# Kernel tuning notes

Measured on AMD Instinct MI355X. Metric: run time of the kernel, lower is better.

## Reference

```python
import jax, jax.numpy as jnp
import numpy as np

DIM = 320; HEADS = 8; DHEAD = 40; CTX_DIM = 768
INNER = HEADS * DHEAD; FF_INNER = 4 * DIM
B = 1; N = 4096; M = 77
SCALE = DHEAD ** -0.5


def setup_inputs() -> dict:
    key = jax.random.key(0)
    ks = jax.random.split(key, 16)
    p = lambda i, shape: jax.random.normal(ks[i], shape, dtype=jnp.float32) * 0.02
    return {
        "x": jax.random.normal(ks[0], (B, N, DIM), dtype=jnp.float32),
        "context": jax.random.normal(ks[1], (B, M, CTX_DIM), dtype=jnp.float32),
        "focused_attention_mask": jax.random.uniform(ks[2], (1, M, M), dtype=jnp.float32),
        "g1": jnp.ones((DIM,), jnp.float32), "b1": jnp.zeros((DIM,), jnp.float32),
        "g2": jnp.ones((DIM,), jnp.float32), "b2": jnp.zeros((DIM,), jnp.float32),
        "g3": jnp.ones((DIM,), jnp.float32), "b3": jnp.zeros((DIM,), jnp.float32),
        "Wq1": p(3, (DIM, INNER)), "Wk1": p(4, (DIM, INNER)), "Wv1": p(5, (DIM, INNER)),
        "Wo1": p(6, (INNER, DIM)), "bo1": jnp.zeros((DIM,), jnp.float32),
        "Wq2": p(7, (DIM, INNER)), "Wk2": p(8, (CTX_DIM, INNER)), "Wv2": p(9, (CTX_DIM, INNER)),
        "Wo2": p(10, (INNER, DIM)), "bo2": jnp.zeros((DIM,), jnp.float32),
        "Wff1": p(11, (DIM, 2 * FF_INNER)), "bff1": jnp.zeros((2 * FF_INNER,), jnp.float32),
        "Wff2": p(12, (FF_INNER, DIM)), "bff2": jnp.zeros((DIM,), jnp.float32),
        "use_fca": 1,
    }


def _ln(x, g, b):
    mu = x.mean(-1, keepdims=True)
    var = jnp.mean((x - mu) ** 2, -1, keepdims=True)
    return (x - mu) * jax.lax.rsqrt(var + 1e-5) * g + b


def _attn(xn, ctx, Wq, Wk, Wv, Wo, bo, fam, use_fca):
    b, n, _ = xn.shape
    heads = lambda t: t.reshape(b, t.shape[1], HEADS, DHEAD).transpose(0, 2, 1, 3)  # b h n d
    q, k, v = heads(xn @ Wq), heads(ctx @ Wk), heads(ctx @ Wv)
    sim = jnp.einsum('bhid,bhjd->bhij', q, k) * SCALE
    if use_fca:
        m = fam.shape[-1]  # fam: [1, m, m], batch must be 1 (repeat_interleave semantics)
        fw = jnp.einsum('bhqk,dk->bhqd', sim[..., :m], fam[0])
        fw = jnp.minimum(jnp.abs(fw), 1.0)
        fw = fw / (jnp.max(fw, axis=-1, keepdims=True) + 1e-6)
        fw = (fw > 0.6).astype(sim.dtype)
        sim = sim.at[..., :m].add((fw - 1.0) * 50.0)
    a = jax.nn.softmax(sim, axis=-1)
    o = jnp.einsum('bhij,bhjd->bhid', a, v).transpose(0, 2, 1, 3).reshape(b, n, INNER)
    return o @ Wo + bo


def reference(x, context, focused_attention_mask,
              g1, b1, g2, b2, g3, b3,
              Wq1, Wk1, Wv1, Wo1, bo1,
              Wq2, Wk2, Wv2, Wo2, bo2,
              Wff1, bff1, Wff2, bff2, use_fca):
    # attn1: self-attention (context=None in original -> use_fca forced to 0)
    h1 = _ln(x, g1, b1)
    x = _attn(h1, h1, Wq1, Wk1, Wv1, Wo1, bo1, None, 0) + x
    # attn2: cross-attention with focused-attention mask
    h2 = _ln(x, g2, b2)
    x = _attn(h2, context, Wq2, Wk2, Wv2, Wo2, bo2, focused_attention_mask, int(use_fca)) + x
    # GEGLU feed-forward
    h3 = _ln(x, g3, b3)
    proj = h3 @ Wff1 + bff1
    a_, gate = jnp.split(proj, 2, axis=-1)
    x = (a_ * jax.nn.gelu(gate, approximate=False)) @ Wff2 + bff2 + x
    return x
```

## Files before the change

kernel.cpp:

```cpp
#include <hip/hip_runtime.h>
#include <math.h>

typedef __bf16 bf16_t;
typedef __bf16 bf16x8 __attribute__((ext_vector_type(8)));
typedef __bf16 bf16x4 __attribute__((ext_vector_type(4)));
typedef float  f32x4  __attribute__((ext_vector_type(4)));
typedef _Float16 f16_t;
typedef _Float16 f16x4 __attribute__((ext_vector_type(4)));
typedef _Float16 f16x8 __attribute__((ext_vector_type(8)));
typedef __fp16 hf16x2 __attribute__((ext_vector_type(2)));

static constexpr float ATT_SCALE = 0.15811388300841897f;
static constexpr float SC2 = 0.22811031f;
static constexpr float LOG2E = 1.4426950408889634f;

__device__ __forceinline__ bf16_t f2b(float f) {
  unsigned u = __float_as_uint(f);
  u = (u + 0x7fffu + ((u >> 16) & 1u)) >> 16;
  unsigned short s = (unsigned short)u;
  bf16_t r;
  *(unsigned short*)&r = s;
  return r;
}
__device__ __forceinline__ float b2f(bf16_t b) {
  unsigned short s = *(const unsigned short*)&b;
  return __uint_as_float(((unsigned)s) << 16);
}
__device__ __forceinline__ void sto(float v, float* p)  { *p = v; }
__device__ __forceinline__ void sto(float v, bf16_t* p) { *p = f2b(v); }
__device__ __forceinline__ unsigned pkh2(float a, float b) {
  hf16x2 h = __builtin_amdgcn_cvt_pkrtz(a, b);
  return *(unsigned*)&h;
}
__device__ __forceinline__ void gl_lds16(const void* g, void* l) {
  __builtin_amdgcn_global_load_lds((const __attribute__((address_space(1))) unsigned*)g,
                                   (__attribute__((address_space(3))) unsigned*)l, 16, 0, 0);
}

__global__ __launch_bounds__(256) void prep_ln_kernel(
    const float* __restrict__ Wq1, const float* __restrict__ Wk1, const float* __restrict__ Wv1,
    const float* __restrict__ Wo1, const float* __restrict__ Wq2,
    const float* __restrict__ Wk2, const float* __restrict__ Wv2, const float* __restrict__ Wo2,
    const float* __restrict__ Wff1, const float* __restrict__ Wff2,
    const float* __restrict__ fam,
    bf16_t* __restrict__ wqkvt, bf16_t* __restrict__ wo1t, float* __restrict__ wkv2t,
    bf16_t* __restrict__ wo2t, bf16_t* __restrict__ wff1t, bf16_t* __restrict__ wff2t,
    bf16_t* __restrict__ wq2th, bf16_t* __restrict__ wq2tl,
    bf16_t* __restrict__ famh, bf16_t* __restrict__ faml,
    bf16_t* __restrict__ zpad,
    const float* __restrict__ x, const float* __restrict__ g1, const float* __restrict__ b1,
    bf16_t* __restrict__ h1b)
{
  const int b = blockIdx.x;
  const int tid = threadIdx.x;

  if (b >= 634) {
    const int bb = b - 634;
    const int lane = tid & 63;
    const int row = bb * 4 + (tid >> 6);
    const float* xr = x + (size_t)row * 320;
    float v[5], s = 0.f, s2 = 0.f;
#pragma unroll
    for (int i = 0; i < 5; i++) { v[i] = xr[lane + i*64]; s += v[i]; s2 += v[i]*v[i]; }
#pragma unroll
    for (int o = 32; o; o >>= 1) { s += __shfl_xor(s, o); s2 += __shfl_xor(s2, o); }
    float mu = s * (1.f/320.f);
    float rs = rsqrtf(fmaxf(s2*(1.f/320.f) - mu*mu, 0.f) + 1e-5f);
#pragma unroll
    for (int i = 0; i < 5; i++) {
      int c = lane + i*64;
      h1b[(size_t)row*320 + c] = f2b((v[i]-mu)*rs*g1[c] + b1[c]);
    }
    return;
  }

  if (b >= 570) {
    for (int idx = (b - 570)*256 + tid; idx < 9216 + 135168; idx += 64*256) {
      if (idx < 9216) {
        int d = idx / 96, k = idx - d*96;
        float v = (d < 77 && k < 77) ? fam[d*77 + k] : 0.f;
        bf16_t h = f2b(v);
        famh[idx] = h;
        faml[idx] = f2b(v - b2f(h));
      } else {
        zpad[idx - 9216] = f2b(0.f);
      }
    }
    return;
  }

  __shared__ float T[64][65];
  const float* src; int S, O, n0, k0, mode;
  float scale = 1.f;
  bf16_t* outb = nullptr; float* outf = nullptr;
  int nadj;

  if (b < 75) {
    int tn = b / 5, tk = b - tn*5;
    n0 = tn*64; k0 = tk*64; S = 320; O = 320; mode = 0; outb = wqkvt;
    if (n0 < 320)      { src = Wq1; nadj = n0;       scale = SC2; }
    else if (n0 < 640) { src = Wk1; nadj = n0 - 320; }
    else               { src = Wv1; nadj = n0 - 640; }
  } else if (b < 100) {
    int b2 = b - 75; int tn = b2 / 5, tk = b2 - tn*5;
    n0 = tn*64; k0 = tk*64; S = 320; O = 320; mode = 0; outb = wo1t; src = Wo1; nadj = n0;
  } else if (b < 220) {
    int b2 = b - 100; int tn = b2 / 12, tk = b2 - tn*12;
    n0 = tn*64; k0 = tk*64; S = 320; O = 768; mode = 1; outf = wkv2t;
    if (n0 < 320) { src = Wk2; nadj = n0; } else { src = Wv2; nadj = n0 - 320; }
  } else if (b < 245) {
    int b2 = b - 220; int tn = b2 / 5, tk = b2 - tn*5;
    n0 = tn*64; k0 = tk*64; S = 320; O = 320; mode = 0; outb = wo2t; src = Wo2; nadj = n0;
  } else if (b < 445) {
    int b2 = b - 245; int tn = b2 / 5, tk = b2 - tn*5;
    n0 = tn*64; k0 = tk*64; S = 2560; O = 320; mode = 0; outb = wff1t; src = Wff1; nadj = n0;
  } else if (b < 545) {
    int b2 = b - 445; int tn = b2 / 20, tk = b2 - tn*20;
    n0 = tn*64; k0 = tk*64; S = 320; O = 1280; mode = 0; outb = wff2t; src = Wff2; nadj = n0;
  } else {
    int b2 = b - 545; int tn = b2 / 5, tk = b2 - tn*5;
    n0 = tn*64; k0 = tk*64; S = 320; O = 320; mode = 2; src = Wq2; nadj = n0;
  }

  const int r4 = tid >> 6;
  const int c  = tid & 63;
  const float* srcp = src + nadj;
#pragma unroll
  for (int i = 0; i < 16; i++) {
    int r = i*4 + r4;
    T[c][r] = srcp[(size_t)(k0 + r)*S + c] * scale;
  }
  __syncthreads();
#pragma unroll
  for (int i = 0; i < 16; i++) {
    int r = i*4 + r4;
    float v = T[r][c];
    size_t oi = (size_t)(n0 + r)*O + k0 + c;
    if (mode == 0) {
      outb[oi] = f2b(v);
    } else if (mode == 1) {
      outf[oi] = v;
    } else {
      bf16_t h = f2b(v);
      wq2th[oi] = h;
      wq2tl[oi] = f2b(v - b2f(h));
    }
  }
}

template<typename OT>
__global__ __launch_bounds__(256) void ln_kernel(
    const float* __restrict__ x, const float* __restrict__ g, const float* __restrict__ b,
    OT* __restrict__ out)
{
  const int lane = threadIdx.x & 63;
  const int row = blockIdx.x * 4 + (threadIdx.x >> 6);
  const float* xr = x + (size_t)row * 320;
  float v[5], s = 0.f, s2 = 0.f;
#pragma unroll
  for (int i = 0; i < 5; i++) { v[i] = xr[lane + i*64]; s += v[i]; s2 += v[i]*v[i]; }
#pragma unroll
  for (int o = 32; o; o >>= 1) { s += __shfl_xor(s, o); s2 += __shfl_xor(s2, o); }
  float mu = s * (1.f/320.f);
  float rs = rsqrtf(fmaxf(s2*(1.f/320.f) - mu*mu, 0.f) + 1e-5f);
#pragma unroll
  for (int i = 0; i < 5; i++) {
    int c = lane + i*64;
    sto((v[i]-mu)*rs*g[c] + b[c], &out[(size_t)row*320 + c]);
  }
}

__global__ __launch_bounds__(256) void ln2_split_kernel(
    const float* __restrict__ x, const float* __restrict__ g, const float* __restrict__ b,
    bf16_t* __restrict__ hi, bf16_t* __restrict__ lo)
{
  const int lane = threadIdx.x & 63;
  const int row = blockIdx.x * 4 + (threadIdx.x >> 6);
  const float* xr = x + (size_t)row * 320;
  float v[5], s = 0.f, s2 = 0.f;
#pragma unroll
  for (int i = 0; i < 5; i++) { v[i] = xr[lane + i*64]; s += v[i]; s2 += v[i]*v[i]; }
#pragma unroll
  for (int o = 32; o; o >>= 1) { s += __shfl_xor(s, o); s2 += __shfl_xor(s2, o); }
  float mu = s * (1.f/320.f);
  float rs = rsqrtf(fmaxf(s2*(1.f/320.f) - mu*mu, 0.f) + 1e-5f);
#pragma unroll
  for (int i = 0; i < 5; i++) {
    int c = lane + i*64;
    float y = (v[i]-mu)*rs*g[c] + b[c];
    bf16_t h = f2b(y);
    hi[(size_t)row*320 + c] = h;
    lo[(size_t)row*320 + c] = f2b(y - b2f(h));
  }
}

__global__ __launch_bounds__(256) void kv2_dot_kernel(
    const float* __restrict__ ctx, const float* __restrict__ wkv2t,
    bf16_t* __restrict__ k2h, bf16_t* __restrict__ k2l, bf16_t* __restrict__ v2t)
{
  __shared__ float4 Bs[16][193];
  const int tid = threadIdx.x;
  const int nb = blockIdx.x % 40, ms = blockIdx.x / 40;
  const int n0 = nb*16;
  for (int e = tid; e < 16*192; e += 256) {
    int row = e / 192, c4 = e - row*192;
    Bs[row][c4] = *(const float4*)(wkv2t + (size_t)(n0+row)*768 + c4*4);
  }
  __syncthreads();
  const int g = tid >> 4, q = tid & 15;
  const int mlo = ms*20;
  const int mhi = (mlo + 20 > 77) ? 77 : mlo + 20;
  for (int m = mlo; m < mhi; m++) {
    const float4* a = (const float4*)(ctx + (size_t)m*768);
    float acc = 0.f;
#pragma unroll
    for (int i = 0; i < 12; i++) {
      float4 av = a[i*16+q], bv = Bs[g][i*16+q];
      acc += av.x*bv.x + av.y*bv.y + av.z*bv.z + av.w*bv.w;
    }
#pragma unroll
    for (int o = 8; o; o >>= 1) acc += __shfl_xor(acc, o);
    if (q == 0) {
      int n = n0 + g;
      if (n < 320) {
        int h = n / 40, d = n - h*40;
        int idx = h*6144 + m*64 + d;
        bf16_t hh = f2b(acc);
        k2h[idx] = hh;
        k2l[idx] = f2b(acc - b2f(hh));
      } else {
        int n2 = n - 320; int h = n2 / 40, d = n2 - h*40;
        v2t[h*4608 + d*96 + m] = f2b(acc);
      }
    }
  }
}

__global__ __launch_bounds__(256) void repack_vt_kernel(
    const bf16_t* __restrict__ qkvb, f16_t* __restrict__ vpack, bf16_t* __restrict__ kpack)
{
  __shared__ f16_t T[64*44];
  const int tid = threadIdx.x;
  const int t0 = blockIdx.x * 64, h = blockIdx.y;
  for (int e = tid; e < 320; e += 256) {
    int t = e / 5, c8 = (e - t*5) * 8;
    bf16x8 v = *(const bf16x8*)(qkvb + (size_t)(t0+t)*960 + 640 + h*40 + c8);
    f16_t* dst = &T[t*44 + c8];
#pragma unroll
    for (int j = 0; j < 8; j++) dst[j] = (f16_t)b2f(v[j]);
  }
  __syncthreads();
  for (int e = tid; e < 3072; e += 256) {
    int dt = e >> 10;
    int r  = e & 1023;
    int g2 = r >> 9, o = r & 511;
    int lane = o >> 3, j = o & 7;
    int qd = lane >> 4, ln = lane & 15;
    int d = dt*16 + ln;
    int key = g2*32 + ((j & 4) ? 16 : 0) + qd*4 + (j & 3);
    float val;
    if (d < 40)       val = (float)T[key*44 + d];
    else if (d == 40) val = 1.0f;
    else              val = 0.0f;
    vpack[(((size_t)h*3 + dt)*128 + (t0 >> 5) + g2)*512 + o] = (f16_t)val;
  }
  for (int e = tid; e < 2560; e += 256) {
    int g = e / 640, o = e - g*640;
    int key = t0 + g*16;
    bf16_t val;
    if (o < 512) {
      int lane = o >> 3, j = o & 7;
      int qd = lane >> 4, ln = lane & 15;
      val = qkvb[(size_t)(key + ln)*960 + 320 + h*40 + qd*8 + j];
    } else {
      int o2 = o - 512; int ln = o2 >> 3, j = o2 & 7;
      val = qkvb[(size_t)(key + ln)*960 + 320 + h*40 + 32 + j];
    }
    kpack[((size_t)h*256 + (t0 >> 4) + g)*640 + o] = val;
  }
}

__global__ __launch_bounds__(512, 4) void flash_self_kernel(
    const bf16_t* __restrict__ qkvb, const bf16_t* __restrict__ kpack,
    const f16_t* __restrict__ vpack,
    bf16_t* __restrict__ o1a)
{
  __shared__ float Red[12288];
  const int tid = threadIdx.x;
  const int w = tid >> 6, lane = tid & 63;
  const int ln = lane & 15, qd = lane >> 4;
  const int qh = w >> 2, kh = w & 3;
  const int h = blockIdx.x & 7;
  const int q0 = (blockIdx.x >> 3) * 64;

  const int kgbase = h*256 + kh*2;
  const int vgbase = h*384 + kh;
  const int lko = lane*8;

  bf16x8 zero8 = {};
  bf16x8 bq[2][2];
#pragma unroll
  for (int nt = 0; nt < 2; nt++) {
    const bf16_t* qp = qkvb + (size_t)(q0 + qh*32 + nt*16 + ln)*960 + h*40;
    bq[nt][0] = *(const bf16x8*)(qp + qd*8);
    bq[nt][1] = (qd == 0) ? *(const bf16x8*)(qp + 32) : zero8;
  }

  f32x4 zero4 = {0.f,0.f,0.f,0.f};
  f32x4 oacc[3][2];
#pragma unroll
  for (int a = 0; a < 3; a++)
#pragma unroll
    for (int b = 0; b < 2; b++) oacc[a][b] = zero4;

#define FS_LOADK(DST, K0)                                                       \
  {                                                                             \
    const bf16_t* kp_ = kpack + ((size_t)kgbase + ((K0) >> 4)) * 640;           \
    DST[0][0] = *(const bf16x8*)(kp_ + lko);                                    \
    DST[0][1] = (qd == 0) ? *(const bf16x8*)(kp_ + 512 + ln*8) : zero8;         \
    DST[1][0] = *(const bf16x8*)(kp_ + 640 + lko);                              \
    DST[1][1] = (qd == 0) ? *(const bf16x8*)(kp_ + 1152 + ln*8) : zero8;        \
  }

#define FS_LOADV(DST, K0)                                                       \
  {                                                                             \
    _Pragma("unroll")                                                           \
    for (int dt_ = 0; dt_ < 3; dt_++)                                           \
      DST[dt_] = *(const f16x8*)(vpack + ((size_t)vgbase + dt_*128 + ((K0) >> 5)) * 512 + lko); \
  }

#define FS_COMPUTE(KA, VA)                                                      \
  {                                                                             \
    __builtin_amdgcn_s_setprio(1);                                              \
    _Pragma("unroll")                                                           \
    for (int nt = 0; nt < 2; nt++) {                                            \
      f32x4 s0 = __builtin_amdgcn_mfma_f32_16x16x32_bf16(KA[0][0], bq[nt][0], zero4, 0,0,0); \
      s0 = __builtin_amdgcn_mfma_f32_16x16x32_bf16(KA[0][1], bq[nt][1], s0, 0,0,0); \
      f32x4 s1 = __builtin_amdgcn_mfma_f32_16x16x32_bf16(KA[1][0], bq[nt][0], zero4, 0,0,0); \
      s1 = __builtin_amdgcn_mfma_f32_16x16x32_bf16(KA[1][1], bq[nt][1], s1, 0,0,0); \
      uint4 u_;                                                                 \
      u_.x = pkh2(__builtin_amdgcn_exp2f(s0[0]), __builtin_amdgcn_exp2f(s0[1])); \
      u_.y = pkh2(__builtin_amdgcn_exp2f(s0[2]), __builtin_amdgcn_exp2f(s0[3])); \
      u_.z = pkh2(__builtin_amdgcn_exp2f(s1[0]), __builtin_amdgcn_exp2f(s1[1])); \
      u_.w = pkh2(__builtin_amdgcn_exp2f(s1[2]), __builtin_amdgcn_exp2f(s1[3])); \
      f16x8 pb = *(f16x8*)&u_;                                                  \
      _Pragma("unroll")                                                         \
      for (int dt = 0; dt < 3; dt++)                                            \
        oacc[dt][nt] = __builtin_amdgcn_mfma_f32_16x16x32_f16(VA[dt], pb, oacc[dt][nt], 0,0,0); \
    }                                                                           \
    __builtin_amdgcn_s_setprio(0);                                              \
  }

  bf16x8 ka[2][2], kb[2][2];
  f16x8 va[3], vb[3];
  FS_LOADK(ka, 0);
  FS_LOADV(va, 0);
#pragma unroll 1
  for (int it = 0; it < 32; it += 2) {
    const int k0 = it*128;
    FS_LOADK(kb, k0 + 128);
    FS_LOADV(vb, k0 + 128);
    FS_COMPUTE(ka, va);
    FS_LOADK(ka, (it + 2 < 32) ? (k0 + 256) : 0);
    FS_LOADV(va, (it + 2 < 32) ? (k0 + 256) : 0);
    FS_COMPUTE(kb, vb);
  }
#undef FS_LOADK
#undef FS_LOADV
#undef FS_COMPUTE

#pragma unroll
  for (int nt = 0; nt < 2; nt++)
#pragma unroll
    for (int dt = 0; dt < 3; dt++)
      *(f32x4*)&Red[((w*2 + nt)*3 + dt)*256 + ln*16 + qd*4] = oacc[dt][nt];
  __syncthreads();
  const int dgrp = tid & 7, lq = (tid >> 3) & 15, ntw = (tid >> 7) & 1, qh2 = tid >> 8;
  float l = Red[(((qh2*4 + 0)*2 + ntw)*3 + 2)*256 + lq*16 + 8]
          + Red[(((qh2*4 + 1)*2 + ntw)*3 + 2)*256 + lq*16 + 8]
          + Red[(((qh2*4 + 2)*2 + ntw)*3 + 2)*256 + lq*16 + 8]
          + Red[(((qh2*4 + 3)*2 + ntw)*3 + 2)*256 + lq*16 + 8];
  float inv = 1.f / l;
  bf16_t* obase = o1a + (size_t)(q0 + qh2*32 + ntw*16 + lq)*320 + h*40;
#pragma unroll
  for (int i = 0; i < 5; i++) {
    int d = dgrp + i*8;
    int dt = d >> 4, dr = d & 15;
    float o = Red[(((qh2*4 + 0)*2 + ntw)*3 + dt)*256 + lq*16 + dr]
            + Red[(((qh2*4 + 1)*2 + ntw)*3 + dt)*256 + lq*16 + dr]
            + Red[(((qh2*4 + 2)*2 + ntw)*3 + dt)*256 + lq*16 + dr]
            + Red[(((qh2*4 + 3)*2 + ntw)*3 + dt)*256 + lq*16 + dr];
    obase[d] = f2b(o * inv);
  }
}

__global__ __launch_bounds__(256) void attn_cross_kernel(
    const float* __restrict__ q2, const bf16_t* __restrict__ k2h, const bf16_t* __restrict__ k2l,
    const bf16_t* __restrict__ famh, const bf16_t* __restrict__ faml,
    const bf16_t* __restrict__ v2t, const int* __restrict__ use_fca,
    bf16_t* __restrict__ o2)
{
  __shared__ bf16_t SMh[4][16*96];
  __shared__ bf16_t SMl[4][16*96];
  __shared__ bf16_t PAs[4][16*96];
  const int tid = threadIdx.x;
  const int w = tid >> 6, lane = tid & 63;
  const int ln = lane & 15, qd = lane >> 4;
  const int h = blockIdx.x & 7;
  const int q0 = (blockIdx.x >> 3)*64 + w*16;
  const int fca = use_fca[0];
  bf16_t* smh = SMh[w];
  bf16_t* sml = SMl[w];
  bf16_t* pa  = PAs[w];

  {
    bf16x4 z = {};
    int q = lane >> 2, c = 80 + (lane & 3)*4;
    *(bf16x4*)&smh[q*96 + c] = z;
    *(bf16x4*)&sml[q*96 + c] = z;
    *(bf16x4*)&pa [q*96 + c] = z;
  }

  bf16x8 zero8 = {};
  bf16x8 aqh0, aql0, aqh1 = zero8, aql1 = zero8;
  {
    const float* qp = q2 + (size_t)(q0 + ln)*320 + h*40;
    float4 v0 = *(const float4*)(qp + qd*8);
    float4 v1 = *(const float4*)(qp + qd*8 + 4);
    float qv[8] = {v0.x,v0.y,v0.z,v0.w,v1.x,v1.y,v1.z,v1.w};
#pragma unroll
    for (int i = 0; i < 8; i++) {
      bf16_t hh = f2b(qv[i]);
      aqh0[i] = hh; aql0[i] = f2b(qv[i] - b2f(hh));
    }
    if (qd == 0) {
      float4 u0 = *(const float4*)(qp + 32);
      float4 u1 = *(const float4*)(qp + 36);
      float uv[8] = {u0.x,u0.y,u0.z,u0.w,u1.x,u1.y,u1.z,u1.w};
#pragma unroll
      for (int i = 0; i < 8; i++) {
        bf16_t hh = f2b(uv[i]);
        aqh1[i] = hh; aql1[i] = f2b(uv[i] - b2f(hh));
      }
    }
  }

  f32x4 zero4 = {0.f,0.f,0.f,0.f};
  float ss[5][4];
  __builtin_amdgcn_s_setprio(1);
#pragma unroll
  for (int nt = 0; nt < 5; nt++) {
    const bf16_t* kb = k2h + ((size_t)h*96 + nt*16 + ln)*64 + qd*8;
    const bf16_t* kl = k2l + ((size_t)h*96 + nt*16 + ln)*64 + qd*8;
    bf16x8 kh0 = *(const bf16x8*)kb;
    bf16x8 kh1 = *(const bf16x8*)(kb + 32);
    bf16x8 kl0 = *(const bf16x8*)kl;
    bf16x8 kl1 = *(const bf16x8*)(kl + 32);
    f32x4 s;
    s = __builtin_amdgcn_mfma_f32_16x16x32_bf16(aqh0, kl0, zero4, 0, 0, 0);
    s = __builtin_amdgcn_mfma_f32_16x16x32_bf16(aql0, kh0, s, 0, 0, 0);
    s = __builtin_amdgcn_mfma_f32_16x16x32_bf16(aqh0, kh0, s, 0, 0, 0);
    s = __builtin_amdgcn_mfma_f32_16x16x32_bf16(aqh1, kl1, s, 0, 0, 0);
    s = __builtin_amdgcn_mfma_f32_16x16x32_bf16(aql1, kh1, s, 0, 0, 0);
    s = __builtin_amdgcn_mfma_f32_16x16x32_bf16(aqh1, kh1, s, 0, 0, 0);
#pragma unroll
    for (int r = 0; r < 4; r++) {
      float sv = s[r] * ATT_SCALE;
      ss[nt][r] = sv;
      bf16_t hh = f2b(sv);
      smh[(qd*4 + r)*96 + nt*16 + ln] = hh;
      sml[(qd*4 + r)*96 + nt*16 + ln] = f2b(sv - b2f(hh));
    }
  }
  __builtin_amdgcn_s_setprio(0);

  f32x4 facc[5];
#pragma unroll
  for (int nt = 0; nt < 5; nt++) facc[nt] = zero4;
  __builtin_amdgcn_s_setprio(1);
#pragma unroll
  for (int c = 0; c < 3; c++) {
    bf16x8 sah = *(const bf16x8*)&smh[ln*96 + c*32 + qd*8];
    bf16x8 sal = *(const bf16x8*)&sml[ln*96 + c*32 + qd*8];
#pragma unroll
    for (int nt = 0; nt < 5; nt++) {
      bf16x8 fh8 = *(const bf16x8*)(famh + ((size_t)(nt*16 + ln))*96 + c*32 + qd*8);
      bf16x8 fl8 = *(const bf16x8*)(faml + ((size_t)(nt*16 + ln))*96 + c*32 + qd*8);
      facc[nt] = __builtin_amdgcn_mfma_f32_16x16x32_bf16(sah, fl8, facc[nt], 0, 0, 0);
      facc[nt] = __builtin_amdgcn_mfma_f32_16x16x32_bf16(sal, fh8, facc[nt], 0, 0, 0);
      facc[nt] = __builtin_amdgcn_mfma_f32_16x16x32_bf16(sah, fh8, facc[nt], 0, 0, 0);
    }
  }
  __builtin_amdgcn_s_setprio(0);

  float pr[5][4];
  if (fca) {
    float fwv[5][4], fm[4];
#pragma unroll
    for (int nt = 0; nt < 5; nt++)
#pragma unroll
      for (int r = 0; r < 4; r++) fwv[nt][r] = fminf(fabsf(facc[nt][r]), 1.f);
#pragma unroll
    for (int r = 0; r < 4; r++) {
      float m = fmaxf(fmaxf(fwv[0][r], fwv[1][r]), fmaxf(fwv[2][r], fmaxf(fwv[3][r], fwv[4][r])));
#pragma unroll
      for (int o = 8; o; o >>= 1) m = fmaxf(m, __shfl_xor(m, o));
      fm[r] = m;
    }
#pragma unroll
    for (int nt = 0; nt < 5; nt++)
#pragma unroll
      for (int r = 0; r < 4; r++) {
        float lg = ss[nt][r] - ((fwv[nt][r] > 0.6f*(fm[r] + 1e-6f)) ? 0.f : 50.f);
        pr[nt][r] = __builtin_amdgcn_exp2f(lg * LOG2E);
      }
  } else {
#pragma unroll
    for (int nt = 0; nt < 5; nt++)
#pragma unroll
      for (int r = 0; r < 4; r++)
        pr[nt][r] = __builtin_amdgcn_exp2f(ss[nt][r] * LOG2E);
  }
  if (ln >= 13) {
#pragma unroll
    for (int r = 0; r < 4; r++) pr[4][r] = 0.f;
  }
  float l_[4] = {0.f,0.f,0.f,0.f};
#pragma unroll
  for (int nt = 0; nt < 5; nt++)
#pragma unroll
    for (int r = 0; r < 4; r++) {
      l_[r] += pr[nt][r];
      pa[(qd*4 + r)*96 + nt*16 + ln] = f2b(pr[nt][r]);
    }
#pragma unroll
  for (int r = 0; r < 4; r++)
#pragma unroll
    for (int o = 8; o; o >>= 1) l_[r] += __shfl_xor(l_[r], o);

  f32x4 oacc[3];
#pragma unroll
  for (int nt = 0; nt < 3; nt++) oacc[nt] = zero4;
  __builtin_amdgcn_s_setprio(1);
#pragma unroll
  for (int c = 0; c < 3; c++) {
    bf16x8 paf = *(const bf16x8*)&pa[ln*96 + c*32 + qd*8];
#pragma unroll
    for (int nt = 0; nt < 3; nt++) {
      bf16x8 vb = *(const bf16x8*)(v2t + ((size_t)h*48 + nt*16 + ln)*96 + c*32 + qd*8);
      oacc[nt] = __builtin_amdgcn_mfma_f32_16x16x32_bf16(paf, vb, oacc[nt], 0, 0, 0);
    }
  }
  __builtin_amdgcn_s_setprio(0);
  float inv[4];
#pragma unroll
  for (int r = 0; r < 4; r++) inv[r] = 1.f / l_[r];
#pragma unroll
  for (int nt = 0; nt < 3; nt++) {
    int d = nt*16 + ln;
    if (d < 40) {
#pragma unroll
      for (int r = 0; r < 4; r++)
        o2[(size_t)(q0 + qd*4 + r)*320 + h*40 + d] = f2b(oacc[nt][r]*inv[r]);
    }
  }
}

template<int OUT_BF16>
__global__ __launch_bounds__(256) void gemm_bf16_kernel(
    const bf16_t* __restrict__ A, const bf16_t* __restrict__ Bt,
    const float* __restrict__ bias, const float* __restrict__ resid,
    void* __restrict__ Cout, int M, int N, int K)
{
  __shared__ __align__(16) bf16_t As[128][64];
  __shared__ __align__(16) bf16_t Bs[64][64];
  const int tid = threadIdx.x;
  const int m0 = blockIdx.x * 128, n0 = blockIdx.y * 64;
  const int w = tid >> 6, lane = tid & 63;
  const int wr = w >> 1, wc = w & 1;
  const int ln = lane & 15, qd = lane >> 4;
  const int lr = lane >> 3, lsw = (lane & 7) ^ lr;
  char* asb = (char*)&As[0][0];
  char* bsb = (char*)&Bs[0][0];
  f32x4 zero = {0.f, 0.f, 0.f, 0.f};
  f32x4 acc[4][2];
#pragma unroll
  for (int a = 0; a < 4; a++)
#pragma unroll
    for (int b = 0; b < 2; b++) acc[a][b] = zero;

  for (int k0 = 0; k0 < K; k0 += 64) {
    __syncthreads();
#pragma unroll
    for (int i = 0; i < 4; i++)
      gl_lds16(A + (size_t)(m0 + (i*4 + w)*8 + lr)*K + k0 + lsw*8, asb + (i*4 + w)*1024);
#pragma unroll
    for (int i = 0; i < 2; i++)
      gl_lds16(Bt + (size_t)(n0 + (i*4 + w)*8 + lr)*K + k0 + lsw*8, bsb + (i*4 + w)*1024);
    __syncthreads();
#pragma unroll
    for (int c = 0; c < 2; c++) {
      const int sa = (((c*4 + qd) ^ (ln & 7))) * 8;
      bf16x8 af[4], bfr[2];
#pragma unroll
      for (int mt = 0; mt < 4; mt++)
        af[mt] = *(const bf16x8*)&As[wr*64 + mt*16 + ln][sa];
#pragma unroll
      for (int nt = 0; nt < 2; nt++)
        bfr[nt] = *(const bf16x8*)&Bs[wc*32 + nt*16 + ln][sa];
#pragma unroll
      for (int mt = 0; mt < 4; mt++)
#pragma unroll
        for (int nt = 0; nt < 2; nt++)
          acc[mt][nt] = __builtin_amdgcn_mfma_f32_16x16x32_bf16(af[mt], bfr[nt], acc[mt][nt], 0, 0, 0);
    }
  }
#pragma unroll
  for (int mt = 0; mt < 4; mt++)
#pragma unroll
    for (int nt = 0; nt < 2; nt++)
#pragma unroll
      for (int r = 0; r < 4; r++) {
        int gm = m0 + wr*64 + mt*16 + qd*4 + r;
        int gn = n0 + wc*32 + nt*16 + ln;
        float v = acc[mt][nt][r];
        if (bias)  v += bias[gn];
        if (resid) v += resid[(size_t)gm*N + gn];
        if (OUT_BF16) sto(v, &((bf16_t*)Cout)[(size_t)gm*N + gn]);
        else          sto(v, &((float*)Cout)[(size_t)gm*N + gn]);
      }
}

template<int OUT_BF16>
__global__ __launch_bounds__(256) void gemm_bf16_32_kernel(
    const bf16_t* __restrict__ A, const bf16_t* __restrict__ Bt,
    const float* __restrict__ bias, const float* __restrict__ resid,
    void* __restrict__ Cout, int M, int N, int K)
{
  __shared__ __align__(16) bf16_t As[32][64];
  __shared__ __align__(16) bf16_t Bs[64][64];
  const int tid = threadIdx.x;
  const int m0 = blockIdx.x * 32, n0 = blockIdx.y * 64;
  const int w = tid >> 6, lane = tid & 63;
  const int wr = w >> 1, wc = w & 1;
  const int ln = lane & 15, qd = lane >> 4;
  const int lr = lane >> 3, lsw = (lane & 7) ^ lr;
  char* asb = (char*)&As[0][0];
  char* bsb = (char*)&Bs[0][0];
  f32x4 zero = {0.f, 0.f, 0.f, 0.f};
  f32x4 acc[2];
  acc[0] = zero; acc[1] = zero;

  for (int k0 = 0; k0 < K; k0 += 64) {
    __syncthreads();
    gl_lds16(A + (size_t)(m0 + w*8 + lr)*K + k0 + lsw*8, asb + w*1024);
#pragma unroll
    for (int i = 0; i < 2; i++)
      gl_lds16(Bt + (size_t)(n0 + (i*4 + w)*8 + lr)*K + k0 + lsw*8, bsb + (i*4 + w)*1024);
    __syncthreads();
#pragma unroll
    for (int c = 0; c < 2; c++) {
      const int sa = (((c*4 + qd) ^ (ln & 7))) * 8;
      bf16x8 af = *(const bf16x8*)&As[wr*16 + ln][sa];
#pragma unroll
      for (int nt = 0; nt < 2; nt++) {
        bf16x8 bfr = *(const bf16x8*)&Bs[wc*32 + nt*16 + ln][sa];
        acc[nt] = __builtin_amdgcn_mfma_f32_16x16x32_bf16(af, bfr, acc[nt], 0, 0, 0);
      }
    }
  }
#pragma unroll
  for (int nt = 0; nt < 2; nt++)
#pragma unroll
    for (int r = 0; r < 4; r++) {
      int gm = m0 + wr*16 + qd*4 + r;
      int gn = n0 + wc*32 + nt*16 + ln;
      float v = acc[nt][r];
      if (bias)  v += bias[gn];
      if (resid) v += resid[(size_t)gm*N + gn];
      if (OUT_BF16) sto(v, &((bf16_t*)Cout)[(size_t)gm*N + gn]);
      else          sto(v, &((float*)Cout)[(size_t)gm*N + gn]);
    }
}

__global__ __launch_bounds__(256) void gemm3_32_kernel(
    const bf16_t* __restrict__ Ah, const bf16_t* __restrict__ Al,
    const bf16_t* __restrict__ Bth, const bf16_t* __restrict__ Btl,
    float* __restrict__ C, int M, int N, int K)
{
  __shared__ bf16_t Ash[32][72];
  __shared__ bf16_t Asl[32][72];
  __shared__ bf16_t Bsh[64][72];
  __shared__ bf16_t Bsl[64][72];
  const int tid = threadIdx.x;
  const int m0 = blockIdx.x * 32, n0 = blockIdx.y * 64;
  const int w = tid >> 6, lane = tid & 63;
  const int wr = w >> 1, wc = w & 1;
  const int ln = lane & 15, qd = lane >> 4;
  f32x4 zero = {0.f, 0.f, 0.f, 0.f};
  f32x4 acc[2];
  acc[0] = zero; acc[1] = zero;

  for (int k0 = 0; k0 < K; k0 += 64) {
    __syncthreads();
    {
      int r = tid >> 3, c8 = (tid & 7) * 8;
      *(bf16x8*)&Ash[r][c8] = *(const bf16x8*)(Ah + (size_t)(m0+r)*K + k0 + c8);
      *(bf16x8*)&Asl[r][c8] = *(const bf16x8*)(Al + (size_t)(m0+r)*K + k0 + c8);
    }
#pragma unroll
    for (int i = 0; i < 2; i++) {
      int vid = tid + i*256;
      int r = vid >> 3, c8 = (vid & 7) * 8;
      *(bf16x8*)&Bsh[r][c8] = *(const bf16x8*)(Bth + (size_t)(n0+r)*K + k0 + c8);
      *(bf16x8*)&Bsl[r][c8] = *(const bf16x8*)(Btl + (size_t)(n0+r)*K + k0 + c8);
    }
    __syncthreads();
#pragma unroll
    for (int c = 0; c < 2; c++) {
      bf16x8 afh = *(const bf16x8*)&Ash[wr*16 + ln][c*32 + qd*8];
      bf16x8 afl = *(const bf16x8*)&Asl[wr*16 + ln][c*32 + qd*8];
#pragma unroll
      for (int nt = 0; nt < 2; nt++) {
        bf16x8 bfh = *(const bf16x8*)&Bsh[wc*32 + nt*16 + ln][c*32 + qd*8];
        bf16x8 bfl = *(const bf16x8*)&Bsl[wc*32 + nt*16 + ln][c*32 + qd*8];
        acc[nt] = __builtin_amdgcn_mfma_f32_16x16x32_bf16(afh, bfl, acc[nt], 0, 0, 0);
        acc[nt] = __builtin_amdgcn_mfma_f32_16x16x32_bf16(afl, bfh, acc[nt], 0, 0, 0);
        acc[nt] = __builtin_amdgcn_mfma_f32_16x16x32_bf16(afh, bfh, acc[nt], 0, 0, 0);
      }
    }
  }
#pragma unroll
  for (int nt = 0; nt < 2; nt++)
#pragma unroll
    for (int r = 0; r < 4; r++) {
      int gm = m0 + wr*16 + qd*4 + r;
      int gn = n0 + wc*32 + nt*16 + ln;
      C[(size_t)gm*N + gn] = acc[nt][r];
    }
}

__global__ __launch_bounds__(256) void gemm_geglu_kernel(
    const bf16_t* __restrict__ A, const bf16_t* __restrict__ Bt,
    const float* __restrict__ bias, bf16_t* __restrict__ gg, int K)
{
  __shared__ __align__(16) bf16_t As[128][64];
  __shared__ __align__(16) bf16_t Ba[64][64];
  __shared__ __align__(16) bf16_t Bg[64][64];
  const int tid = threadIdx.x;
  const int m0 = blockIdx.x * 128, n0 = blockIdx.y * 64;
  const int w = tid >> 6, lane = tid & 63;
  const int wr = w >> 1, wc = w & 1;
  const int ln = lane & 15, qd = lane >> 4;
  const int lr = lane >> 3, lsw = (lane & 7) ^ lr;
  char* asb = (char*)&As[0][0];
  char* bab = (char*)&Ba[0][0];
  char* bgb = (char*)&Bg[0][0];
  f32x4 zero = {0.f, 0.f, 0.f, 0.f};
  f32x4 acca[4][2], accg[4][2];
#pragma unroll
  for (int a = 0; a < 4; a++)
#pragma unroll
    for (int b = 0; b < 2; b++) { acca[a][b] = zero; accg[a][b] = zero; }

  for (int k0 = 0; k0 < K; k0 += 64) {
    __syncthreads();
#pragma unroll
    for (int i = 0; i < 4; i++)
      gl_lds16(A + (size_t)(m0 + (i*4 + w)*8 + lr)*K + k0 + lsw*8, asb + (i*4 + w)*1024);
#pragma unroll
    for (int i = 0; i < 2; i++) {
      gl_lds16(Bt + (size_t)(n0 + (i*4 + w)*8 + lr)*K + k0 + lsw*8, bab + (i*4 + w)*1024);
      gl_lds16(Bt + (size_t)(n0 + 1280 + (i*4 + w)*8 + lr)*K + k0 + lsw*8, bgb + (i*4 + w)*1024);
    }
    __syncthreads();
#pragma unroll
    for (int c = 0; c < 2; c++) {
      const int sa = (((c*4 + qd) ^ (ln & 7))) * 8;
      bf16x8 af[4], ba[2], bg[2];
#pragma unroll
      for (int mt = 0; mt < 4; mt++)
        af[mt] = *(const bf16x8*)&As[wr*64 + mt*16 + ln][sa];
#pragma unroll
      for (int nt = 0; nt < 2; nt++) {
        ba[nt] = *(const bf16x8*)&Ba[wc*32 + nt*16 + ln][sa];
        bg[nt] = *(const bf16x8*)&Bg[wc*32 + nt*16 + ln][sa];
      }
#pragma unroll
      for (int mt = 0; mt < 4; mt++)
#pragma unroll
        for (int nt = 0; nt < 2; nt++) {
          acca[mt][nt] = __builtin_amdgcn_mfma_f32_16x16x32_bf16(af[mt], ba[nt], acca[mt][nt], 0, 0, 0);
          accg[mt][nt] = __builtin_amdgcn_mfma_f32_16x16x32_bf16(af[mt], bg[nt], accg[mt][nt], 0, 0, 0);
        }
    }
  }
#pragma unroll
  for (int mt = 0; mt < 4; mt++)
#pragma unroll
    for (int nt = 0; nt < 2; nt++)
#pragma unroll
      for (int r = 0; r < 4; r++) {
        int gm = m0 + wr*64 + mt*16 + qd*4 + r;
        int gn = n0 + wc*32 + nt*16 + ln;
        float va = acca[mt][nt][r] + bias[gn];
        float vg = accg[mt][nt][r] + bias[1280 + gn];
        float ge = 0.5f * vg * (1.f + erff(vg * 0.70710678118654752f));
        gg[(size_t)gm*1280 + gn] = f2b(va * ge);
      }
}

extern "C" void kernel_launch(void* const* d_in, const int* in_sizes, int n_in,
                              void* d_out, int out_size, void* d_ws, size_t ws_size,
                              hipStream_t stream)
{
  const float* x    = (const float*)d_in[0];
  const float* ctx  = (const float*)d_in[1];
  const float* fam  = (const float*)d_in[2];
  const float* g1   = (const float*)d_in[3];
  const float* b1   = (const float*)d_in[4];
  const float* g2   = (const float*)d_in[5];
  const float* b2   = (const float*)d_in[6];
  const float* g3   = (const float*)d_in[7];
  const float* b3   = (const float*)d_in[8];
  const float* Wq1  = (const float*)d_in[9];
  const float* Wk1  = (const float*)d_in[10];
  const float* Wv1  = (const float*)d_in[11];
  const float* Wo1  = (const float*)d_in[12];
  const float* bo1  = (const float*)d_in[13];
  const float* Wq2  = (const float*)d_in[14];
  const float* Wk2  = (const float*)d_in[15];
  const float* Wv2  = (const float*)d_in[16];
  const float* Wo2  = (const float*)d_in[17];
  const float* bo2  = (const float*)d_in[18];
  const float* Wff1 = (const float*)d_in[19];
  const float* bff1 = (const float*)d_in[20];
  const float* Wff2 = (const float*)d_in[21];
  const float* bff2 = (const float*)d_in[22];
  const int*   ufca = (const int*)d_in[23];

  char* ws = (char*)d_ws;
  bf16_t* qkvb = (bf16_t*)(ws + 0);
  f16_t*  vpack = (f16_t*)(ws + 7864320);
  bf16_t* kpack = (bf16_t*)(ws + 11010048);
  bf16_t* h1b  = (bf16_t*)(ws + 13631488);
  bf16_t* h2hi = (bf16_t*)(ws + 16252928);
  bf16_t* h2lo = (bf16_t*)(ws + 18874368);
  float*  x2   = (float*)(ws + 21495808);
  float*  q2   = (float*)(ws + 26738688);
  bf16_t* o1a  = (bf16_t*)(ws + 26738688);
  bf16_t* o2   = (bf16_t*)(ws + 32178688);
  float*  x3   = (float*)(ws + 34800128);
  bf16_t* h3b  = (bf16_t*)(ws + 40043008);
  bf16_t* wqkvt = (bf16_t*)(ws + 42664448);
  bf16_t* wo1t  = (bf16_t*)(ws + 43278848);
  float*  wkv2t = (float*)(ws + 43483648);
  bf16_t* wo2t  = (bf16_t*)(ws + 45449728);
  bf16_t* wff1t = (bf16_t*)(ws + 45654528);
  bf16_t* wff2t = (bf16_t*)(ws + 47292928);
  bf16_t* wq2th = (bf16_t*)(ws + 48374272);
  bf16_t* wq2tl = (bf16_t*)(ws + 48579072);
  bf16_t* famh  = (bf16_t*)(ws + 48783872);
  bf16_t* faml  = (bf16_t*)(ws + 48802304);
  bf16_t* k2h   = (bf16_t*)(ws + 48820736);
  bf16_t* k2l   = (bf16_t*)(ws + 48919040);
  bf16_t* v2t   = (bf16_t*)(ws + 49017344);
  bf16_t* gg   = (bf16_t*)(ws + 21495808);

  float* xout = (float*)d_out;

  prep_ln_kernel<<<1658, 256, 0, stream>>>(Wq1, Wk1, Wv1, Wo1, Wq2, Wk2, Wv2, Wo2, Wff1, Wff2, fam,
                                           wqkvt, wo1t, wkv2t, wo2t, wff1t, wff2t, wq2th, wq2tl,
                                           famh, faml, k2h, x, g1, b1, h1b);
  gemm_bf16_kernel<1><<<dim3(32,15), 256, 0, stream>>>(h1b, wqkvt, nullptr, nullptr, qkvb, 4096, 960, 320);
  repack_vt_kernel<<<dim3(64,8), 256, 0, stream>>>(qkvb, vpack, kpack);
  flash_self_kernel<<<512, 512, 0, stream>>>(qkvb, kpack, vpack, o1a);
  gemm_bf16_32_kernel<0><<<dim3(128,5), 256, 0, stream>>>(o1a, wo1t, bo1, x, x2, 4096, 320, 320);
  ln2_split_kernel<<<1024, 256, 0, stream>>>(x2, g2, b2, h2hi, h2lo);
  gemm3_32_kernel<<<dim3(128,5), 256, 0, stream>>>(h2hi, h2lo, wq2th, wq2tl, q2, 4096, 320, 320);
  kv2_dot_kernel<<<160, 256, 0, stream>>>(ctx, wkv2t, k2h, k2l, v2t);
  attn_cross_kernel<<<512, 256, 0, stream>>>(q2, k2h, k2l, famh, faml, v2t, ufca, o2);
  gemm_bf16_32_kernel<0><<<dim3(128,5), 256, 0, stream>>>(o2, wo2t, bo2, x2, x3, 4096, 320, 320);
  ln_kernel<bf16_t><<<1024, 256, 0, stream>>>(x3, g3, b3, h3b);
  gemm_geglu_kernel<<<dim3(32,20), 256, 0, stream>>>(h3b, wff1t, bff1, gg, 320);
  gemm_bf16_32_kernel<0><<<dim3(128,5), 256, 0, stream>>>(gg, wff2t, bff2, x3, xout, 4096, 320, 1280);
}
```

Measured before the change: 254.3 us.

## Double-buffer LDS tiles in bf16 GEMM kernels to overlap loads with MFMA

New measurement: 250.2 us. No clear change (-1.6%).

```diff
diff --git a/kernel.cpp b/kernel.cpp
--- a/kernel.cpp
+++ b/kernel.cpp
@@ -572,16 +572,14 @@
     const float* __restrict__ bias, const float* __restrict__ resid,
     void* __restrict__ Cout, int M, int N, int K)
 {
-  __shared__ __align__(16) bf16_t As[128][64];
-  __shared__ __align__(16) bf16_t Bs[64][64];
+  __shared__ __align__(16) bf16_t As[2][128][64];
+  __shared__ __align__(16) bf16_t Bs[2][64][64];
   const int tid = threadIdx.x;
   const int m0 = blockIdx.x * 128, n0 = blockIdx.y * 64;
   const int w = tid >> 6, lane = tid & 63;
   const int wr = w >> 1, wc = w & 1;
   const int ln = lane & 15, qd = lane >> 4;
   const int lr = lane >> 3, lsw = (lane & 7) ^ lr;
-  char* asb = (char*)&As[0][0];
-  char* bsb = (char*)&Bs[0][0];
   f32x4 zero = {0.f, 0.f, 0.f, 0.f};
   f32x4 acc[4][2];
 #pragma unroll
@@ -589,32 +587,43 @@
 #pragma unroll
     for (int b = 0; b < 2; b++) acc[a][b] = zero;
 
-  for (int k0 = 0; k0 < K; k0 += 64) {
-    __syncthreads();
-#pragma unroll
-    for (int i = 0; i < 4; i++)
-      gl_lds16(A + (size_t)(m0 + (i*4 + w)*8 + lr)*K + k0 + lsw*8, asb + (i*4 + w)*1024);
-#pragma unroll
-    for (int i = 0; i < 2; i++)
-      gl_lds16(Bt + (size_t)(n0 + (i*4 + w)*8 + lr)*K + k0 + lsw*8, bsb + (i*4 + w)*1024);
-    __syncthreads();
+#define GB_STAGE(BI, KK)                                                          \
+  {                                                                               \
+    char* asb_ = (char*)&As[BI][0][0];                                            \
+    char* bsb_ = (char*)&Bs[BI][0][0];                                            \
+    _Pragma("unroll")                                                             \
+    for (int i = 0; i < 4; i++)                                                   \
+      gl_lds16(A + (size_t)(m0 + (i*4 + w)*8 + lr)*K + (KK) + lsw*8, asb_ + (i*4 + w)*1024); \
+    _Pragma("unroll")                                                             \
+    for (int i = 0; i < 2; i++)                                                   \
+      gl_lds16(Bt + (size_t)(n0 + (i*4 + w)*8 + lr)*K + (KK) + lsw*8, bsb_ + (i*4 + w)*1024); \
+  }
+
+  const int NT = K >> 6;
+  GB_STAGE(0, 0)
+  __syncthreads();
+  for (int t = 0; t < NT; t++) {
+    if (t + 1 < NT) GB_STAGE((t + 1) & 1, (t + 1) * 64)
+    const int bi = t & 1;
 #pragma unroll
     for (int c = 0; c < 2; c++) {
       const int sa = (((c*4 + qd) ^ (ln & 7))) * 8;
       bf16x8 af[4], bfr[2];
 #pragma unroll
       for (int mt = 0; mt < 4; mt++)
-        af[mt] = *(const bf16x8*)&As[wr*64 + mt*16 + ln][sa];
+        af[mt] = *(const bf16x8*)&As[bi][wr*64 + mt*16 + ln][sa];
 #pragma unroll
       for (int nt = 0; nt < 2; nt++)
-        bfr[nt] = *(const bf16x8*)&Bs[wc*32 + nt*16 + ln][sa];
+        bfr[nt] = *(const bf16x8*)&Bs[bi][wc*32 + nt*16 + ln][sa];
 #pragma unroll
       for (int mt = 0; mt < 4; mt++)
 #pragma unroll
         for (int nt = 0; nt < 2; nt++)
           acc[mt][nt] = __builtin_amdgcn_mfma_f32_16x16x32_bf16(af[mt], bfr[nt], acc[mt][nt], 0, 0, 0);
     }
-  }
+    __syncthreads();
+  }
+#undef GB_STAGE
 #pragma unroll
   for (int mt = 0; mt < 4; mt++)
 #pragma unroll
@@ -637,38 +646,47 @@
     const float* __restrict__ bias, const float* __restrict__ resid,
     void* __restrict__ Cout, int M, int N, int K)
 {
-  __shared__ __align__(16) bf16_t As[32][64];
-  __shared__ __align__(16) bf16_t Bs[64][64];
+  __shared__ __align__(16) bf16_t As[2][32][64];
+  __shared__ __align__(16) bf16_t Bs[2][64][64];
   const int tid = threadIdx.x;
   const int m0 = blockIdx.x * 32, n0 = blockIdx.y * 64;
   const int w = tid >> 6, lane = tid & 63;
   const int wr = w >> 1, wc = w & 1;
   const int ln = lane & 15, qd = lane >> 4;
   const int lr = lane >> 3, lsw = (lane & 7) ^ lr;
-  char* asb = (char*)&As[0][0];
-  char* bsb = (char*)&Bs[0][0];
   f32x4 zero = {0.f, 0.f, 0.f, 0.f};
   f32x4 acc[2];
   acc[0] = zero; acc[1] = zero;
 
-  for (int k0 = 0; k0 < K; k0 += 64) {
-    __syncthreads();
-    gl_lds16(A + (size_t)(m0 + w*8 + lr)*K + k0 + lsw*8, asb + w*1024);
-#pragma unroll
-    for (int i = 0; i < 2; i++)
-      gl_lds16(Bt + (size_t)(n0 + (i*4 + w)*8 + lr)*K + k0 + lsw*8, bsb + (i*4 + w)*1024);
-    __syncthreads();
+#define GB32_STAGE(BI, KK)                                                        \
+  {                                                                               \
+    char* asb_ = (char*)&As[BI][0][0];                                            \
+    char* bsb_ = (char*)&Bs[BI][0][0];                                            \
+    gl_lds16(A + (size_t)(m0 + w*8 + lr)*K + (KK) + lsw*8, asb_ + w*1024);        \
+    _Pragma("unroll")                                                             \
+    for (int i = 0; i < 2; i++)                                                   \
+      gl_lds16(Bt + (size_t)(n0 + (i*4 + w)*8 + lr)*K + (KK) + lsw*8, bsb_ + (i*4 + w)*1024); \
+  }
+
+  const int NT = K >> 6;
+  GB32_STAGE(0, 0)
+  __syncthreads();
+  for (int t = 0; t < NT; t++) {
+    if (t + 1 < NT) GB32_STAGE((t + 1) & 1, (t + 1) * 64)
+    const int bi = t & 1;
 #pragma unroll
     for (int c = 0; c < 2; c++) {
       const int sa = (((c*4 + qd) ^ (ln & 7))) * 8;
-      bf16x8 af = *(const bf16x8*)&As[wr*16 + ln][sa];
+      bf16x8 af = *(const bf16x8*)&As[bi][wr*16 + ln][sa];
 #pragma unroll
       for (int nt = 0; nt < 2; nt++) {
-        bf16x8 bfr = *(const bf16x8*)&Bs[wc*32 + nt*16 + ln][sa];
+        bf16x8 bfr = *(const bf16x8*)&Bs[bi][wc*32 + nt*16 + ln][sa];
         acc[nt] = __builtin_amdgcn_mfma_f32_16x16x32_bf16(af, bfr, acc[nt], 0, 0, 0);
       }
     }
-  }
+    __syncthreads();
+  }
+#undef GB32_STAGE
 #pragma unroll
   for (int nt = 0; nt < 2; nt++)
 #pragma unroll
```
